# Kernel optimization log

Hardware: AMD Instinct MI355X
Metric: run time of the kernel (lower is better)

Reference implementation:

```python
import jax, jax.numpy as jnp
import numpy as np

FRS = np.array([1, 2, 4, 8, 16, 25, 36, 50, 75], dtype=np.float32)
N_EXPERTS = len(FRS)
N = 1048576
DIMS = [(4, 32), (32, 32), (32, 64), (64, 64)]


def setup_inputs() -> dict:
    key = jax.random.key(0)
    ks = jax.random.split(key, 2 + 8)
    # features: col 0 = framerate drawn from the known framerate set, cols 1:5 = affinity feats
    fr_idx = jax.random.randint(ks[0], (N,), 0, N_EXPERTS)
    framerates = jnp.asarray(FRS)[fr_idx]
    aff = jax.random.normal(ks[1], (N, 4), dtype=jnp.float32)
    features = jnp.concatenate([framerates[:, None], aff], axis=1)
    # stacked per-expert MLP params (torch Linear: y = x @ W.T + b; store W as [in,out])
    params = {}
    scale = 0.1
    for li, (din, dout) in enumerate(DIMS):
        params[f"W{li+1}"] = scale * jax.random.normal(ks[2 + 2 * li], (N_EXPERTS, din, dout), dtype=jnp.float32)
        params[f"b{li+1}"] = scale * jax.random.normal(ks[3 + 2 * li], (N_EXPERTS, dout), dtype=jnp.float32)
    return {"features": features, **params}


def _expert_mlp(x, W1, b1, W2, b2, W3, b3, W4, b4):
    h = jax.nn.relu(x @ W1 + b1)
    h = jax.nn.relu(h @ W2 + b2)
    h = jax.nn.relu(h @ W3 + b3)
    return h @ W4 + b4  # [N, 64]


def reference(features, W1, b1, W2, b2, W3, b3, W4, b4):
    frs = jnp.asarray(FRS)
    framerates = features[:, 0]
    x = features[:, 1:]  # [N, 4] (ignore_appr=False)
    # nearest-framerate expert index (argmin picks first min, matching find_index)
    k = jnp.argmin(jnp.abs(framerates[:, None] - frs[None, :]), axis=1)  # [N]
    pred = jnp.zeros(features.shape[0], dtype=features.dtype)
    for e in range(N_EXPERTS):  # fixed, small expert set
        out_e = _expert_mlp(x, W1[e], b1[e], W2[e], b2[e], W3[e], b3[e], W4[e], b4[e])
        pred = jnp.where(k == e, out_e.sum(axis=1), pred)
    return pred
```

## Files before the change

### kernel.cpp

```cpp
#include <hip/hip_runtime.h>
#include <stdint.h>

#define NEXP 9
#define FTHR 512
#define RPH 2
#define SBLK (FTHR * RPH)
#define PADSLK (SBLK + NEXP * 32)
#define MAXT 48
#define TBL_BYTES 7936
#define CLS_STRIDE 136

typedef float f32x4 __attribute__((ext_vector_type(4)));
typedef float f32x16 __attribute__((ext_vector_type(16)));
typedef _Float16 f16x8 __attribute__((ext_vector_type(8)));

struct alignas(16) I4 { int a, b, c, d; };
struct alignas(64) Q4 { f32x4 a, b, c, d; };

__device__ __forceinline__ int pk(float a, float b) {
    return __builtin_bit_cast(int, __builtin_amdgcn_cvt_pkrtz(a, b));
}
__device__ __forceinline__ int pkh(float a, float b) {
    int p = pk(a, b);
    int r;
    int z = 0;
    asm("v_pk_max_f16 %0, %1, %2" : "=v"(r) : "v"(p), "v"(z));
    return r;
}
__device__ __forceinline__ f32x16 zero16() {
    f32x16 z;
#pragma unroll
    for (int r = 0; r < 16; ++r) z[r] = 0.f;
    return z;
}

__device__ __forceinline__ int expert_of(float fr) {
    return (fr > 1.5f) + (fr > 3.f) + (fr > 6.f) + (fr > 12.f)
         + (fr > 20.5f) + (fr > 30.5f) + (fr > 43.f) + (fr > 62.5f);
}

__global__ __launch_bounds__(256) void k_prep(const float* __restrict__ W1, const float* __restrict__ b1,
                                              const float* __restrict__ W2, const float* __restrict__ b2,
                                              const float* __restrict__ W3, const float* __restrict__ b3,
                                              const float* __restrict__ W4, const float* __restrict__ b4,
                                              char* __restrict__ tab) {
    int e = blockIdx.x;
    int tid = threadIdx.x;
    char* T = tab + (size_t)e * TBL_BYTES;

    __shared__ float psum[64][4];
    __shared__ float rs2[64];
    __shared__ float b4s_s;
    {
        int row = tid >> 2, q = tid & 3;
        const float* w = W4 + (size_t)e * 4096 + row * 64 + q * 16;
        f32x4 a = *(const f32x4*)(w + 0), b = *(const f32x4*)(w + 4);
        f32x4 c = *(const f32x4*)(w + 8), d = *(const f32x4*)(w + 12);
        psum[row][q] = (a.x + a.y + a.z + a.w) + (b.x + b.y + b.z + b.w)
                     + (c.x + c.y + c.z + c.w) + (d.x + d.y + d.z + d.w);
    }
    __syncthreads();
    if (tid < 64) {
        int l = tid, g = l >> 5, m = l & 31;
        rs2[l] = psum[l][0] + psum[l][1] + psum[l][2] + psum[l][3];
        float bp = b4[e * 64 + l];
#pragma unroll
        for (int d = 1; d < 64; d <<= 1) bp += __shfl_xor(bp, d, 64);
        if (l == 0) b4s_s = bp;

        {
            f16x8 v;
#pragma unroll
            for (int ei = 0; ei < 8; ++ei) {
                int k = g * 8 + ei;
                float w = (k < 4) ? W1[e * 128 + k * 32 + m] : (k == 4 ? b1[e * 32 + m] : 0.f);
                v[ei] = (_Float16)w;
            }
            *(f16x8*)(T + 0 * 1024 + l * 16) = v;
        }
#pragma unroll
        for (int kf = 0; kf < 2; ++kf) {
            f16x8 v;
#pragma unroll
            for (int ei = 0; ei < 8; ++ei) {
                int row = kf * 16 + (ei & 3) + 8 * (ei >> 2) + 4 * g;
                v[ei] = (_Float16)W2[e * 1024 + row * 32 + m];
            }
            *(f16x8*)(T + (1 + kf) * 1024 + l * 16) = v;
        }
#pragma unroll
        for (int t = 0; t < 2; ++t)
#pragma unroll
            for (int kf = 0; kf < 2; ++kf) {
                f16x8 v;
#pragma unroll
                for (int ei = 0; ei < 8; ++ei) {
                    int row = kf * 16 + (ei & 3) + 8 * (ei >> 2) + 4 * g;
                    v[ei] = (_Float16)W3[e * 2048 + row * 64 + t * 32 + m];
                }
                *(f16x8*)(T + (3 + t * 2 + kf) * 1024 + l * 16) = v;
            }
    }
    __syncthreads();
    if (tid < 32) {
        int g = tid >> 4, r = tid & 15;
        int row = (r & 3) + 8 * (r >> 2) + 4 * g;
        float* C = (float*)(T + 7168);
        C[0 * 32 + tid] = b2[e * 32 + row];
        C[1 * 32 + tid] = b3[e * 64 + row];
        C[2 * 32 + tid] = b3[e * 64 + 32 + row];
        if (tid == 0) C[96] = b4s_s;
        {
            int f = tid >> 3, gg = (tid >> 2) & 1, j = tid & 3;
            int t = f >> 1, h = f & 1;
            int e0 = 2 * j, e1 = 2 * j + 1;
            int r0 = t * 32 + h * 16 + (e0 & 3) + 8 * (e0 >> 2) + 4 * gg;
            int r1 = t * 32 + h * 16 + (e1 & 3) + 8 * (e1 >> 2) + 4 * gg;
            C[100 + tid] = __builtin_bit_cast(float, pk(rs2[r0], rs2[r1]));
        }
    }
}

__global__ __launch_bounds__(FTHR, 6) void k_main(const float* __restrict__ feat, int n,
                                                  const char* __restrict__ tab,
                                                  float* __restrict__ out) {
    __shared__ __align__(16) uint2 bx[PADSLK];
    __shared__ unsigned short bidx[PADSLK];
    __shared__ __align__(16) float cls[NEXP * CLS_STRIDE];
    __shared__ int lcnt[NEXP];
    __shared__ int pbase[NEXP];
    __shared__ int wbase[RPH][8][NEXP];
    __shared__ unsigned char tile_e[MAXT];
    __shared__ short tile_s[MAXT];
    __shared__ unsigned char tile_v[MAXT];
    __shared__ int nt_s;

    int bid = blockIdx.x, tid = threadIdx.x;
    int wid = tid >> 6, lane = tid & 63, g = lane >> 5, m = lane & 31;
    int gbase = bid * SBLK;

    if (tid < NEXP) lcnt[tid] = 0;
    {
        uint2 z = {0u, 0u};
#pragma unroll
        for (int q = 0; q < 3; ++q) {
            int o = q * FTHR + tid;
            if (o < PADSLK) bx[o] = z;
        }
    }
    {
        const float* tf = (const float*)tab;
        for (int idx = tid; idx < NEXP * CLS_STRIDE; idx += FTHR) {
            int e = idx / CLS_STRIDE, o = idx - e * CLS_STRIDE;
            cls[idx] = tf[e * (TBL_BYTES / 4) + 1792 + o];
        }
    }
    __syncthreads();

    int kk[RPH], rk[RPH];
    uint2 xw[RPH];
#pragma unroll
    for (int r = 0; r < RPH; ++r) {
        int i = gbase + r * FTHR + tid;
        int k = -1;
        uint2 w = {0u, 0u};
        if (i < n) {
            const float* f = feat + (size_t)i * 5;
            k = expert_of(f[0]);
            w.x = (unsigned)pk(f[1], f[2]);
            w.y = (unsigned)pk(f[3], f[4]);
        }
        kk[r] = k; xw[r] = w;
        unsigned long long myM = 0;
#pragma unroll
        for (int e = 0; e < NEXP; ++e) {
            unsigned long long mm = __ballot(k == e);
            if (k == e) myM = mm;
            if (lane == 0) {
                int c = __popcll(mm);
                wbase[r][wid][e] = c ? atomicAdd(&lcnt[e], c) : 0;
            }
        }
        rk[r] = __popcll(myM & ((1ull << lane) - 1ull));
    }
    __syncthreads();

    if (wid == 0) {
        int e = lane;
        int c = (e < NEXP) ? lcnt[e] : 0;
        int ntl = (c + 31) >> 5;
        int padc = ntl << 5;
        int sp = padc, st = ntl;
#pragma unroll
        for (int d = 1; d < 16; d <<= 1) {
            int a = __shfl_up(sp, d, 64);
            int b = __shfl_up(st, d, 64);
            if (lane >= d) { sp += a; st += b; }
        }
        if (e < NEXP) {
            int pb = sp - padc, tb = st - ntl;
            pbase[e] = pb;
            for (int j = 0; j < ntl; ++j) {
                tile_e[tb + j] = (unsigned char)e;
                tile_s[tb + j] = (short)(pb + j * 32);
                int v = c - j * 32;
                tile_v[tb + j] = (unsigned char)(v > 32 ? 32 : v);
            }
            if (e == NEXP - 1) nt_s = st;
        }
    }
    __syncthreads();

#pragma unroll
    for (int r = 0; r < RPH; ++r) {
        int k = kk[r];
        if (k >= 0) {
            int slot = pbase[k] + wbase[r][wid][k] + rk[r];
            bx[slot] = xw[r];
            bidx[slot] = (unsigned short)(r * FTHR + tid);
        }
    }
    __syncthreads();

    int nt = nt_s;
    int t0 = (wid * nt) >> 3, t1 = ((wid + 1) * nt) >> 3;
    int cur_e = -1;
    f16x8 A1 = {}, A2a = {}, A2b = {}, A30a = {}, A30b = {}, A31a = {}, A31b = {};
    const float* Cc = cls;
    const float* A4p = cls;
    float b4v = 0.f;
    for (int t = t0; t < t1; ++t) {
        int e = __builtin_amdgcn_readfirstlane((int)tile_e[t]);
        if (e != cur_e) {
            cur_e = e;
            const char* T = tab + (size_t)e * TBL_BYTES;
            A1 = *(const f16x8*)(T + 0 * 1024 + lane * 16);
            A2a = *(const f16x8*)(T + 1 * 1024 + lane * 16);
            A2b = *(const f16x8*)(T + 2 * 1024 + lane * 16);
            A30a = *(const f16x8*)(T + 3 * 1024 + lane * 16);
            A30b = *(const f16x8*)(T + 4 * 1024 + lane * 16);
            A31a = *(const f16x8*)(T + 5 * 1024 + lane * 16);
            A31b = *(const f16x8*)(T + 6 * 1024 + lane * 16);
            Cc = cls + e * CLS_STRIDE + g * 16;
            A4p = cls + e * CLS_STRIDE + 100 + g * 4;
            b4v = cls[e * CLS_STRIDE + 96];
        }
        auto ldC = [&](int mat) -> f32x16 {
            const float* c = Cc + mat * 32;
            Q4 q;
            q.a = *(const f32x4*)(c + 0);
            q.b = *(const f32x4*)(c + 4);
            q.c = *(const f32x4*)(c + 8);
            q.d = *(const f32x4*)(c + 12);
            return __builtin_bit_cast(f32x16, q);
        };
        auto ldA4 = [&](int f) -> f16x8 {
            return __builtin_bit_cast(f16x8, *(const f32x4*)(A4p + f * 8));
        };

        int s = tile_s[t], v = tile_v[t];
        uint2 xv = bx[s + m];

        I4 b1i = {g ? 0 : (int)xv.x, g ? 0 : (int)xv.y, g ? 0 : 0x3C00, 0};
        f16x8 B1 = __builtin_bit_cast(f16x8, b1i);

        f32x16 d1 = __builtin_amdgcn_mfma_f32_32x32x16_f16(A1, B1, zero16(), 0, 0, 0);
        I4 p0 = {pkh(d1[0], d1[1]), pkh(d1[2], d1[3]), pkh(d1[4], d1[5]), pkh(d1[6], d1[7])};
        I4 p1 = {pkh(d1[8], d1[9]), pkh(d1[10], d1[11]), pkh(d1[12], d1[13]), pkh(d1[14], d1[15])};
        f16x8 B2a = __builtin_bit_cast(f16x8, p0);
        f16x8 B2b = __builtin_bit_cast(f16x8, p1);

        f32x16 d2 = __builtin_amdgcn_mfma_f32_32x32x16_f16(A2a, B2a, ldC(0), 0, 0, 0);
        d2 = __builtin_amdgcn_mfma_f32_32x32x16_f16(A2b, B2b, d2, 0, 0, 0);
        I4 q0 = {pkh(d2[0], d2[1]), pkh(d2[2], d2[3]), pkh(d2[4], d2[5]), pkh(d2[6], d2[7])};
        I4 q1 = {pkh(d2[8], d2[9]), pkh(d2[10], d2[11]), pkh(d2[12], d2[13]), pkh(d2[14], d2[15])};
        f16x8 B3a = __builtin_bit_cast(f16x8, q0);
        f16x8 B3b = __builtin_bit_cast(f16x8, q1);

        f32x16 d4;
        {
            f32x16 d3 = __builtin_amdgcn_mfma_f32_32x32x16_f16(A30a, B3a, ldC(1), 0, 0, 0);
            d3 = __builtin_amdgcn_mfma_f32_32x32x16_f16(A30b, B3b, d3, 0, 0, 0);
            I4 u0 = {pkh(d3[0], d3[1]), pkh(d3[2], d3[3]), pkh(d3[4], d3[5]), pkh(d3[6], d3[7])};
            I4 u1 = {pkh(d3[8], d3[9]), pkh(d3[10], d3[11]), pkh(d3[12], d3[13]), pkh(d3[14], d3[15])};
            d4 = __builtin_amdgcn_mfma_f32_32x32x16_f16(ldA4(0), __builtin_bit_cast(f16x8, u0), zero16(), 0, 0, 0);
            d4 = __builtin_amdgcn_mfma_f32_32x32x16_f16(ldA4(1), __builtin_bit_cast(f16x8, u1), d4, 0, 0, 0);
        }
        {
            f32x16 d3 = __builtin_amdgcn_mfma_f32_32x32x16_f16(A31a, B3a, ldC(2), 0, 0, 0);
            d3 = __builtin_amdgcn_mfma_f32_32x32x16_f16(A31b, B3b, d3, 0, 0, 0);
            I4 u0 = {pkh(d3[0], d3[1]), pkh(d3[2], d3[3]), pkh(d3[4], d3[5]), pkh(d3[6], d3[7])};
            I4 u1 = {pkh(d3[8], d3[9]), pkh(d3[10], d3[11]), pkh(d3[12], d3[13]), pkh(d3[14], d3[15])};
            d4 = __builtin_amdgcn_mfma_f32_32x32x16_f16(ldA4(2), __builtin_bit_cast(f16x8, u0), d4, 0, 0, 0);
            d4 = __builtin_amdgcn_mfma_f32_32x32x16_f16(ldA4(3), __builtin_bit_cast(f16x8, u1), d4, 0, 0, 0);
        }
        if (!g && m < v) out[gbase + (int)bidx[s + m]] = d4[0] + b4v;
    }
}

__global__ __launch_bounds__(256) void k_fallback(const float* __restrict__ feat,
                                                  const float* __restrict__ W1, const float* __restrict__ b1,
                                                  const float* __restrict__ W2, const float* __restrict__ b2,
                                                  const float* __restrict__ W3, const float* __restrict__ b3,
                                                  const float* __restrict__ W4, const float* __restrict__ b4,
                                                  float* __restrict__ out, int n) {
    int i = blockIdx.x * 256 + threadIdx.x;
    if (i >= n) return;
    const float* f = feat + (size_t)i * 5;
    int e = expert_of(f[0]);
    float x0 = f[1], x1 = f[2], x2 = f[3], x3 = f[4];
    float h1[32], h2[32], h3[64];
    for (int j = 0; j < 32; ++j) {
        float a = b1[e * 32 + j];
        a += x0 * W1[e * 128 + 0 * 32 + j];
        a += x1 * W1[e * 128 + 1 * 32 + j];
        a += x2 * W1[e * 128 + 2 * 32 + j];
        a += x3 * W1[e * 128 + 3 * 32 + j];
        h1[j] = fmaxf(a, 0.f);
    }
    for (int j = 0; j < 32; ++j) h2[j] = b2[e * 32 + j];
    for (int i2 = 0; i2 < 32; ++i2)
        for (int j = 0; j < 32; ++j) h2[j] += h1[i2] * W2[e * 1024 + i2 * 32 + j];
    for (int j = 0; j < 32; ++j) h2[j] = fmaxf(h2[j], 0.f);
    for (int j = 0; j < 64; ++j) h3[j] = b3[e * 64 + j];
    for (int i2 = 0; i2 < 32; ++i2)
        for (int j = 0; j < 64; ++j) h3[j] += h2[i2] * W3[e * 2048 + i2 * 64 + j];
    float pred = 0.f;
    for (int o = 0; o < 64; ++o) pred += b4[e * 64 + o];
    for (int j = 0; j < 64; ++j) {
        float rsum = 0.f;
        for (int o = 0; o < 64; ++o) rsum += W4[e * 4096 + j * 64 + o];
        pred += fmaxf(h3[j], 0.f) * rsum;
    }
    out[i] = pred;
}

extern "C" void kernel_launch(void* const* d_in, const int* in_sizes, int n_in,
                              void* d_out, int out_size, void* d_ws, size_t ws_size,
                              hipStream_t stream) {
    const float* feat = (const float*)d_in[0];
    const float* W1 = (const float*)d_in[1];
    const float* b1 = (const float*)d_in[2];
    const float* W2 = (const float*)d_in[3];
    const float* b2 = (const float*)d_in[4];
    const float* W3 = (const float*)d_in[5];
    const float* b3 = (const float*)d_in[6];
    const float* W4 = (const float*)d_in[7];
    const float* b4 = (const float*)d_in[8];
    float* out = (float*)d_out;
    int n = in_sizes[0] / 5;

    const size_t need = (size_t)NEXP * TBL_BYTES;

    if (ws_size >= need) {
        char* tab = (char*)d_ws;
        k_prep<<<NEXP, 256, 0, stream>>>(W1, b1, W2, b2, W3, b3, W4, b4, tab);
        int nb = (n + SBLK - 1) / SBLK;
        k_main<<<nb, FTHR, 0, stream>>>(feat, n, tab, out);
    } else {
        k_fallback<<<(n + 255) / 256, 256, 0, stream>>>(feat, W1, b1, W2, b2, W3, b3, W4, b4, out, n);
    }
}
```

Measured before the change: 33.93 us.

## Process two independent tile streams per wave and double rows per block

```diff
diff --git a/kernel.cpp b/kernel.cpp
--- a/kernel.cpp
+++ b/kernel.cpp
@@ -3,10 +3,10 @@
 
 #define NEXP 9
 #define FTHR 512
-#define RPH 2
+#define RPH 4
 #define SBLK (FTHR * RPH)
 #define PADSLK (SBLK + NEXP * 32)
-#define MAXT 48
+#define MAXT 80
 #define TBL_BYTES 7936
 #define CLS_STRIDE 136
 
@@ -121,9 +121,9 @@
     }
 }
 
-__global__ __launch_bounds__(FTHR, 6) void k_main(const float* __restrict__ feat, int n,
-                                                  const char* __restrict__ tab,
-                                                  float* __restrict__ out) {
+__global__ __launch_bounds__(FTHR) void k_main(const float* __restrict__ feat, int n,
+                                               const char* __restrict__ tab,
+                                               float* __restrict__ out) {
     __shared__ __align__(16) uint2 bx[PADSLK];
     __shared__ unsigned short bidx[PADSLK];
     __shared__ __align__(16) float cls[NEXP * CLS_STRIDE];
@@ -143,7 +143,7 @@
     {
         uint2 z = {0u, 0u};
 #pragma unroll
-        for (int q = 0; q < 3; ++q) {
+        for (int q = 0; q < 5; ++q) {
             int o = q * FTHR + tid;
             if (o < PADSLK) bx[o] = z;
         }
@@ -224,27 +224,23 @@
 
     int nt = nt_s;
     int t0 = (wid * nt) >> 3, t1 = ((wid + 1) * nt) >> 3;
-    int cur_e = -1;
-    f16x8 A1 = {}, A2a = {}, A2b = {}, A30a = {}, A30b = {}, A31a = {}, A31b = {};
-    const float* Cc = cls;
-    const float* A4p = cls;
-    float b4v = 0.f;
-    for (int t = t0; t < t1; ++t) {
-        int e = __builtin_amdgcn_readfirstlane((int)tile_e[t]);
-        if (e != cur_e) {
-            cur_e = e;
-            const char* T = tab + (size_t)e * TBL_BYTES;
-            A1 = *(const f16x8*)(T + 0 * 1024 + lane * 16);
-            A2a = *(const f16x8*)(T + 1 * 1024 + lane * 16);
-            A2b = *(const f16x8*)(T + 2 * 1024 + lane * 16);
-            A30a = *(const f16x8*)(T + 3 * 1024 + lane * 16);
-            A30b = *(const f16x8*)(T + 4 * 1024 + lane * 16);
-            A31a = *(const f16x8*)(T + 5 * 1024 + lane * 16);
-            A31b = *(const f16x8*)(T + 6 * 1024 + lane * 16);
-            Cc = cls + e * CLS_STRIDE + g * 16;
-            A4p = cls + e * CLS_STRIDE + 100 + g * 4;
-            b4v = cls[e * CLS_STRIDE + 96];
-        }
+    int len = t1 - t0;
+    int half = (len + 1) >> 1;
+
+    int curA = -1, curB = -1;
+    f16x8 Aa[7], Ab[7];
+    const float *CcA = cls, *A4A = cls, *CcB = cls, *A4B = cls;
+    float b4A = 0.f, b4B = 0.f;
+
+    auto reload = [&](int e, f16x8* A, const float*& Cc, const float*& A4p, float& b4v) {
+        const char* T = tab + (size_t)e * TBL_BYTES;
+#pragma unroll
+        for (int c = 0; c < 7; ++c) A[c] = *(const f16x8*)(T + c * 1024 + lane * 16);
+        Cc = cls + e * CLS_STRIDE + g * 16;
+        A4p = cls + e * CLS_STRIDE + 100 + g * 4;
+        b4v = cls[e * CLS_STRIDE + 96];
+    };
+    auto run_tile = [&](const f16x8* A, const float* Cc, const float* A4p, uint2 xv) -> float {
         auto ldC = [&](int mat) -> f32x16 {
             const float* c = Cc + mat * 32;
             Q4 q;
@@ -257,21 +253,15 @@
         auto ldA4 = [&](int f) -> f16x8 {
             return __builtin_bit_cast(f16x8, *(const f32x4*)(A4p + f * 8));
         };
-
-        int s = tile_s[t], v = tile_v[t];
-        uint2 xv = bx[s + m];
-
         I4 b1i = {g ? 0 : (int)xv.x, g ? 0 : (int)xv.y, g ? 0 : 0x3C00, 0};
         f16x8 B1 = __builtin_bit_cast(f16x8, b1i);
 
-        f32x16 d1 = __builtin_amdgcn_mfma_f32_32x32x16_f16(A1, B1, zero16(), 0, 0, 0);
+        f32x16 d1 = __builtin_amdgcn_mfma_f32_32x32x16_f16(A[0], B1, zero16(), 0, 0, 0);
         I4 p0 = {pkh(d1[0], d1[1]), pkh(d1[2], d1[3]), pkh(d1[4], d1[5]), pkh(d1[6], d1[7])};
         I4 p1 = {pkh(d1[8], d1[9]), pkh(d1[10], d1[11]), pkh(d1[12], d1[13]), pkh(d1[14], d1[15])};
-        f16x8 B2a = __builtin_bit_cast(f16x8, p0);
-        f16x8 B2b = __builtin_bit_cast(f16x8, p1);
-
-        f32x16 d2 = __builtin_amdgcn_mfma_f32_32x32x16_f16(A2a, B2a, ldC(0), 0, 0, 0);
-        d2 = __builtin_amdgcn_mfma_f32_32x32x16_f16(A2b, B2b, d2, 0, 0, 0);
+
+        f32x16 d2 = __builtin_amdgcn_mfma_f32_32x32x16_f16(A[1], __builtin_bit_cast(f16x8, p0), ldC(0), 0, 0, 0);
+        d2 = __builtin_amdgcn_mfma_f32_32x32x16_f16(A[2], __builtin_bit_cast(f16x8, p1), d2, 0, 0, 0);
         I4 q0 = {pkh(d2[0], d2[1]), pkh(d2[2], d2[3]), pkh(d2[4], d2[5]), pkh(d2[6], d2[7])};
         I4 q1 = {pkh(d2[8], d2[9]), pkh(d2[10], d2[11]), pkh(d2[12], d2[13]), pkh(d2[14], d2[15])};
         f16x8 B3a = __builtin_bit_cast(f16x8, q0);
@@ -279,22 +269,45 @@
 
         f32x16 d4;
         {
-            f32x16 d3 = __builtin_amdgcn_mfma_f32_32x32x16_f16(A30a, B3a, ldC(1), 0, 0, 0);
-            d3 = __builtin_amdgcn_mfma_f32_32x32x16_f16(A30b, B3b, d3, 0, 0, 0);
+            f32x16 d3 = __builtin_amdgcn_mfma_f32_32x32x16_f16(A[3], B3a, ldC(1), 0, 0, 0);
+            d3 = __builtin_amdgcn_mfma_f32_32x32x16_f16(A[4], B3b, d3, 0, 0, 0);
             I4 u0 = {pkh(d3[0], d3[1]), pkh(d3[2], d3[3]), pkh(d3[4], d3[5]), pkh(d3[6], d3[7])};
             I4 u1 = {pkh(d3[8], d3[9]), pkh(d3[10], d3[11]), pkh(d3[12], d3[13]), pkh(d3[14], d3[15])};
             d4 = __builtin_amdgcn_mfma_f32_32x32x16_f16(ldA4(0), __builtin_bit_cast(f16x8, u0), zero16(), 0, 0, 0);
             d4 = __builtin_amdgcn_mfma_f32_32x32x16_f16(ldA4(1), __builtin_bit_cast(f16x8, u1), d4, 0, 0, 0);
         }
         {
-            f32x16 d3 = __builtin_amdgcn_mfma_f32_32x32x16_f16(A31a, B3a, ldC(2), 0, 0, 0);
-            d3 = __builtin_amdgcn_mfma_f32_32x32x16_f16(A31b, B3b, d3, 0, 0, 0);
+            f32x16 d3 = __builtin_amdgcn_mfma_f32_32x32x16_f16(A[5], B3a, ldC(2), 0, 0, 0);
+            d3 = __builtin_amdgcn_mfma_f32_32x32x16_f16(A[6], B3b, d3, 0, 0, 0);
             I4 u0 = {pkh(d3[0], d3[1]), pkh(d3[2], d3[3]), pkh(d3[4], d3[5]), pkh(d3[6], d3[7])};
             I4 u1 = {pkh(d3[8], d3[9]), pkh(d3[10], d3[11]), pkh(d3[12], d3[13]), pkh(d3[14], d3[15])};
             d4 = __builtin_amdgcn_mfma_f32_32x32x16_f16(ldA4(2), __builtin_bit_cast(f16x8, u0), d4, 0, 0, 0);
             d4 = __builtin_amdgcn_mfma_f32_32x32x16_f16(ldA4(3), __builtin_bit_cast(f16x8, u1), d4, 0, 0, 0);
         }
-        if (!g && m < v) out[gbase + (int)bidx[s + m]] = d4[0] + b4v;
+        return d4[0];
+    };
+
+    for (int j = 0; j < half; ++j) {
+        int ta = t0 + j;
+        int tb = t0 + half + j;
+        bool hasB = tb < t1;
+        if (!hasB) tb = ta;
+
+        int ea = __builtin_amdgcn_readfirstlane((int)tile_e[ta]);
+        int eb = __builtin_amdgcn_readfirstlane((int)tile_e[tb]);
+        if (ea != curA) { curA = ea; reload(ea, Aa, CcA, A4A, b4A); }
+        if (eb != curB) { curB = eb; reload(eb, Ab, CcB, A4B, b4B); }
+
+        int sa = tile_s[ta], va = tile_v[ta];
+        int sb = tile_s[tb], vb = hasB ? tile_v[tb] : 0;
+        uint2 xva = bx[sa + m];
+        uint2 xvb = bx[sb + m];
+
+        float ra = run_tile(Aa, CcA, A4A, xva);
+        float rb = run_tile(Ab, CcB, A4B, xvb);
+
+        if (!g && m < va) out[gbase + (int)bidx[sa + m]] = ra + b4A;
+        if (!g && m < vb) out[gbase + (int)bidx[sb + m]] = rb + b4B;
     }
 }
 
```

Result: slower. 42.91 us (+26.5%).
